# Optimization experiments

Hardware: AMD Instinct MI355X
Metric: run time of the kernel (lower is better)

The kernel has to match this reference:

```python
import jax, jax.numpy as jnp
import numpy as np

N_NODES = 50000
N_EDGES = 600000
HIDDEN = 128


def _sage_conv(x, src, dst, W_l, W_r, b):
    """PyG SAGEConv with mean aggregation:
    out_i = W_l @ mean_{j in N(i)} x_j + W_r @ x_i + b
    src/dst: [E] edge endpoints (message flows src -> dst).
    """
    msg = x[src]  # [E, d] gather
    agg = jax.ops.segment_sum(msg, dst, num_segments=N_NODES)  # [N, d]
    cnt = jax.ops.segment_sum(jnp.ones((src.shape[0],), x.dtype), dst,
                              num_segments=N_NODES)  # [N]
    mean = agg / jnp.maximum(cnt, 1.0)[:, None]
    return mean @ W_l.T + x @ W_r.T + b


def setup_inputs() -> dict:
    key = jax.random.key(0)
    ks = jax.random.split(key, 12)
    x = jax.random.normal(ks[0], (N_NODES, HIDDEN), dtype=jnp.float32)
    edge_index = jax.random.randint(ks[1], (2, N_EDGES), 0, N_NODES, dtype=jnp.int64)
    scale = 1.0 / np.sqrt(HIDDEN)
    inp = {"x": x, "edge_index": edge_index}
    for i, layer in enumerate(["1", "2", "3"]):
        inp["Wl" + layer] = jax.random.uniform(ks[2 + 3 * i], (HIDDEN, HIDDEN),
                                               minval=-scale, maxval=scale, dtype=jnp.float32)
        inp["Wr" + layer] = jax.random.uniform(ks[3 + 3 * i], (HIDDEN, HIDDEN),
                                               minval=-scale, maxval=scale, dtype=jnp.float32)
        inp["b" + layer] = jax.random.uniform(ks[4 + 3 * i], (HIDDEN,),
                                              minval=-scale, maxval=scale, dtype=jnp.float32)
    return inp


def reference(x, edge_index, Wl1, Wr1, b1, Wl2, Wr2, b2, Wl3, Wr3, b3):
    src, dst = edge_index[0], edge_index[1]
    h = jax.nn.relu(_sage_conv(x, src, dst, Wl1, Wr1, b1))
    h = _sage_conv(h, src, dst, Wl2, Wr2, b2)
    h = _sage_conv(h, src, dst, Wl3, Wr3, b3)
    return h
```

## Files before the change

### kernel.cpp

```cpp
#include <hip/hip_runtime.h>
#include <hip/hip_bf16.h>

#define N_NODES 50000
#define N_EDGES 600000
#define HID 128

typedef __attribute__((ext_vector_type(8))) short s8v;
typedef __attribute__((ext_vector_type(8))) unsigned short u8v;
typedef __attribute__((ext_vector_type(4))) float f4v;

__device__ __forceinline__ unsigned short f2bf(float x) {
    unsigned u = __float_as_uint(x);
    unsigned r = u + 0x7FFFu + ((u >> 16) & 1u);
    return (unsigned short)(r >> 16);
}
__device__ __forceinline__ float bf2f(unsigned short u) {
    return __uint_as_float((unsigned)u << 16);
}
__device__ __forceinline__ void split_bf(float x, unsigned short& hi, unsigned short& lo) {
    hi = f2bf(x);
    lo = f2bf(x - bf2f(hi));
}

__device__ __forceinline__ int detect_m64(const void* edges) {
    const int* p = (const int*)edges;
    int lane = threadIdx.x & 63;
    unsigned long long nz = __ballot(p[2 * lane + 1] != 0);
    return (nz == 0ULL) ? 1 : 0;
}

__device__ __forceinline__ int edge_at(const void* edges, int mode64, long long idx) {
    return mode64 ? (int)((const long long*)edges)[idx] : ((const int*)edges)[idx];
}

__global__ __launch_bounds__(256) void prep(
    const void* __restrict__ edges, const float* __restrict__ x,
    const float* __restrict__ m0, const float* __restrict__ m1,
    const float* __restrict__ m2, const float* __restrict__ m3,
    const float* __restrict__ m4, const float* __restrict__ m5,
    int* __restrict__ deg,
    unsigned short* __restrict__ whi, unsigned short* __restrict__ wlo,
    unsigned short* __restrict__ xhi, unsigned short* __restrict__ xlo) {
    const int EB  = (N_EDGES + 255) / 256;
    const int WCV = (6 * HID * HID + 255) / 256;
    const int b = blockIdx.x;
    if (b < EB) {
        int m = detect_m64(edges);
        int e = b * 256 + threadIdx.x;
        if (e >= N_EDGES) return;
        int d = edge_at(edges, m, (long long)N_EDGES + e);
        if ((unsigned)d < (unsigned)N_NODES) atomicAdd(&deg[d], 1);
    } else if (b < EB + WCV) {
        int idx = (b - EB) * 256 + threadIdx.x;
        if (idx >= 6 * HID * HID) return;
        int mat = idx >> 14, off = idx & 16383;
        const float* src = mat == 0 ? m0 : mat == 1 ? m1 : mat == 2 ? m2
                         : mat == 3 ? m3 : mat == 4 ? m4 : m5;
        unsigned short h, l;
        split_bf(src[off], h, l);
        whi[idx] = h; wlo[idx] = l;
    } else {
        const int n4 = (N_NODES * HID) / 4;
        int i = (b - EB - WCV) * 256 + threadIdx.x;
        if (i >= n4) return;
        float4 v = ((const float4*)x)[i];
        ushort4 h, l;
        split_bf(v.x, h.x, l.x);
        split_bf(v.y, h.y, l.y);
        split_bf(v.z, h.z, l.z);
        split_bf(v.w, h.w, l.w);
        ((ushort4*)xhi)[i] = h;
        ((ushort4*)xlo)[i] = l;
    }
}

__global__ void scan_block(const int* __restrict__ deg, int* __restrict__ offs,
                           int* __restrict__ blocksum) {
    __shared__ int sm[256];
    int i = blockIdx.x * 256 + threadIdx.x;
    int v = (i < N_NODES) ? deg[i] : 0;
    sm[threadIdx.x] = v;
    __syncthreads();
    #pragma unroll
    for (int s = 1; s < 256; s <<= 1) {
        int t = (threadIdx.x >= (unsigned)s) ? sm[threadIdx.x - s] : 0;
        __syncthreads();
        sm[threadIdx.x] += t;
        __syncthreads();
    }
    if (i < N_NODES) offs[i] = sm[threadIdx.x] - v;
    if (threadIdx.x == 255) blocksum[blockIdx.x] = sm[255];
}

__global__ void scan_add(int* __restrict__ offs, int* __restrict__ cursor,
                         const int* __restrict__ blocksum, int nblocks) {
    __shared__ int sm[256];
    int t = threadIdx.x;
    int bv = (t < nblocks) ? blocksum[t] : 0;
    sm[t] = (t < (int)blockIdx.x) ? bv : 0;
    __syncthreads();
    #pragma unroll
    for (int s = 128; s > 0; s >>= 1) {
        if (t < s) sm[t] += sm[t + s];
        __syncthreads();
    }
    int prefix = sm[0];
    int i = blockIdx.x * 256 + t;
    if (i < N_NODES) {
        int o = offs[i] + prefix;
        offs[i] = o;
        cursor[i] = o;
    }
    if ((int)blockIdx.x == nblocks - 1 && t == 0)
        offs[N_NODES] = prefix + blocksum[nblocks - 1];
}

__global__ void fill_csr(const void* __restrict__ edges,
                         int* __restrict__ cursor, int* __restrict__ csr) {
    int m = detect_m64(edges);
    int e = blockIdx.x * 256 + threadIdx.x;
    if (e >= N_EDGES) return;
    int d = edge_at(edges, m, (long long)N_EDGES + e);
    int s = edge_at(edges, m, (long long)e);
    if ((unsigned)d >= (unsigned)N_NODES || (unsigned)s >= (unsigned)N_NODES) return;
    int pos = atomicAdd(&cursor[d], 1);
    csr[pos] = s;
}

__global__ __launch_bounds__(256) void aggregate_bf16(const unsigned short* __restrict__ h,
                                                      const int* __restrict__ offs,
                                                      const int* __restrict__ csr,
                                                      unsigned short* __restrict__ mhi,
                                                      unsigned short* __restrict__ mlo) {
    const int sub  = threadIdx.x & 15;
    const int node = blockIdx.x * 16 + (threadIdx.x >> 4);
    if (node >= N_NODES) return;
    const int beg = offs[node], end = offs[node + 1];
    float a[8] = {0.f, 0.f, 0.f, 0.f, 0.f, 0.f, 0.f, 0.f};
    int p = beg;
    for (; p + 8 <= end; p += 8) {
        int s0 = csr[p],     s1 = csr[p + 1], s2 = csr[p + 2], s3 = csr[p + 3];
        int s4 = csr[p + 4], s5 = csr[p + 5], s6 = csr[p + 6], s7 = csr[p + 7];
        u8v v0 = *(const u8v*)(h + (size_t)s0 * HID + sub * 8);
        u8v v1 = *(const u8v*)(h + (size_t)s1 * HID + sub * 8);
        u8v v2 = *(const u8v*)(h + (size_t)s2 * HID + sub * 8);
        u8v v3 = *(const u8v*)(h + (size_t)s3 * HID + sub * 8);
        u8v v4 = *(const u8v*)(h + (size_t)s4 * HID + sub * 8);
        u8v v5 = *(const u8v*)(h + (size_t)s5 * HID + sub * 8);
        u8v v6 = *(const u8v*)(h + (size_t)s6 * HID + sub * 8);
        u8v v7 = *(const u8v*)(h + (size_t)s7 * HID + sub * 8);
        #pragma unroll
        for (int j = 0; j < 8; ++j)
            a[j] += ((bf2f(v0[j]) + bf2f(v1[j])) + (bf2f(v2[j]) + bf2f(v3[j])))
                  + ((bf2f(v4[j]) + bf2f(v5[j])) + (bf2f(v6[j]) + bf2f(v7[j])));
    }
    if (p + 4 <= end) {
        int s0 = csr[p], s1 = csr[p + 1], s2 = csr[p + 2], s3 = csr[p + 3];
        u8v v0 = *(const u8v*)(h + (size_t)s0 * HID + sub * 8);
        u8v v1 = *(const u8v*)(h + (size_t)s1 * HID + sub * 8);
        u8v v2 = *(const u8v*)(h + (size_t)s2 * HID + sub * 8);
        u8v v3 = *(const u8v*)(h + (size_t)s3 * HID + sub * 8);
        #pragma unroll
        for (int j = 0; j < 8; ++j)
            a[j] += (bf2f(v0[j]) + bf2f(v1[j])) + (bf2f(v2[j]) + bf2f(v3[j]));
        p += 4;
    }
    for (; p < end; ++p) {
        int s = csr[p];
        u8v v = *(const u8v*)(h + (size_t)s * HID + sub * 8);
        #pragma unroll
        for (int j = 0; j < 8; ++j) a[j] += bf2f(v[j]);
    }
    const float inv = 1.0f / fmaxf((float)(end - beg), 1.0f);
    u8v hh, ll;
    #pragma unroll
    for (int j = 0; j < 8; ++j) {
        unsigned short hj, lj;
        split_bf(a[j] * inv, hj, lj);
        hh[j] = hj; ll[j] = lj;
    }
    *(u8v*)(mhi + (size_t)node * HID + sub * 8) = hh;
    *(u8v*)(mlo + (size_t)node * HID + sub * 8) = ll;
}

template <int RELU, int FINAL>
__global__ __launch_bounds__(256) void sage_mfma(
    const unsigned short* __restrict__ Mhi, const unsigned short* __restrict__ Mlo,
    const unsigned short* __restrict__ Hhi, const unsigned short* __restrict__ Hlo,
    const unsigned short* __restrict__ Whi, const unsigned short* __restrict__ Wlo,
    const float* __restrict__ bias,
    unsigned short* __restrict__ ohi, unsigned short* __restrict__ olo,
    float* __restrict__ of32) {
    __shared__ short BhS[128 * 72];
    __shared__ short BlS[128 * 72];
    const int tid = threadIdx.x;
    const int wave = tid >> 6, lane = tid & 63;
    const int mIdx = lane & 15, q = lane >> 4;
    const int wrow = (wave & 1) * 64, wcol = (wave >> 1) * 64;
    const int rowBase = blockIdx.x * 128;

    size_t aoff[4];
    #pragma unroll
    for (int t = 0; t < 4; ++t) {
        int node = rowBase + wrow + t * 16 + mIdx;
        if (node > N_NODES - 1) node = N_NODES - 1;
        aoff[t] = (size_t)node * HID + q * 8;
    }

    const int bcol = tid & 127;
    const int bseg = (tid >> 7) * 32;

    f4v acc[4][4];
    #pragma unroll
    for (int a = 0; a < 4; ++a)
        #pragma unroll
        for (int b = 0; b < 4; ++b) acc[a][b] = (f4v){0.f, 0.f, 0.f, 0.f};

    s8v Ah[2][4], Al[2][4];
    auto loadA = [&](int i, int buf) {
        const unsigned short* ah_ = (i < 4) ? Mhi : Hhi;
        const unsigned short* al_ = (i < 4) ? Mlo : Hlo;
        const int kc = (i & 3) * 32;
        #pragma unroll
        for (int t = 0; t < 4; ++t) {
            Ah[buf][t] = *(const s8v*)(ah_ + aoff[t] + kc);
            Al[buf][t] = *(const s8v*)(al_ + aoff[t] + kc);
        }
    };

    loadA(0, 0);
    for (int panel = 0; panel < 4; ++panel) {
        const int ph = panel >> 1;
        const int kb = (panel & 1) * 64;
        const unsigned short* Wh_ = Whi + ph * HID * HID;
        const unsigned short* Wl_ = Wlo + ph * HID * HID;
        __syncthreads();
        {
            const unsigned short* sh = Wh_ + bcol * HID + kb + bseg;
            const unsigned short* sl = Wl_ + bcol * HID + kb + bseg;
            short* dh = BhS + bcol * 72 + bseg;
            short* dl = BlS + bcol * 72 + bseg;
            #pragma unroll
            for (int j = 0; j < 4; ++j) {
                *(s8v*)(dh + j * 8) = *(const s8v*)(sh + j * 8);
                *(s8v*)(dl + j * 8) = *(const s8v*)(sl + j * 8);
            }
        }
        __syncthreads();
        #pragma unroll
        for (int c = 0; c < 2; ++c) {
            const int i = panel * 2 + c;
            if (i < 7) loadA(i + 1, (i + 1) & 1);
            const int kc2 = c * 32;
            s8v Bh_f[4], Bl_f[4];
            #pragma unroll
            for (int nt = 0; nt < 4; ++nt) {
                const int a = (wcol + nt * 16 + mIdx) * 72 + kc2 + q * 8;
                Bh_f[nt] = *(const s8v*)(BhS + a);
                Bl_f[nt] = *(const s8v*)(BlS + a);
            }
            const int buf = i & 1;
            #pragma unroll
            for (int mt = 0; mt < 4; ++mt)
                #pragma unroll
                for (int nt = 0; nt < 4; ++nt) {
                    acc[mt][nt] = __builtin_amdgcn_mfma_f32_16x16x32_bf16(
                        Ah[buf][mt], Bh_f[nt], acc[mt][nt], 0, 0, 0);
                    acc[mt][nt] = __builtin_amdgcn_mfma_f32_16x16x32_bf16(
                        Al[buf][mt], Bh_f[nt], acc[mt][nt], 0, 0, 0);
                    acc[mt][nt] = __builtin_amdgcn_mfma_f32_16x16x32_bf16(
                        Ah[buf][mt], Bl_f[nt], acc[mt][nt], 0, 0, 0);
                }
        }
    }

    float bv[4];
    #pragma unroll
    for (int nt = 0; nt < 4; ++nt) bv[nt] = bias[wcol + nt * 16 + mIdx];

    #pragma unroll
    for (int mt = 0; mt < 4; ++mt)
        #pragma unroll
        for (int r = 0; r < 4; ++r) {
            int node = rowBase + wrow + mt * 16 + q * 4 + r;
            if (node < N_NODES) {
                #pragma unroll
                for (int nt = 0; nt < 4; ++nt) {
                    int feat = wcol + nt * 16 + mIdx;
                    float v = acc[mt][nt][r] + bv[nt];
                    if (RELU) v = fmaxf(v, 0.f);
                    size_t oidx = (size_t)node * HID + feat;
                    if (FINAL) {
                        of32[oidx] = v;
                    } else {
                        unsigned short hh, ll;
                        split_bf(v, hh, ll);
                        ohi[oidx] = hh;
                        olo[oidx] = ll;
                    }
                }
            }
        }
}

extern "C" void kernel_launch(void* const* d_in, const int* in_sizes, int n_in,
                              void* d_out, int out_size, void* d_ws, size_t ws_size,
                              hipStream_t stream) {
    const float* x   = (const float*)d_in[0];
    const void* edges = d_in[1];
    const float* Wl1 = (const float*)d_in[2];
    const float* Wr1 = (const float*)d_in[3];
    const float* b1  = (const float*)d_in[4];
    const float* Wl2 = (const float*)d_in[5];
    const float* Wr2 = (const float*)d_in[6];
    const float* b2  = (const float*)d_in[7];
    const float* Wl3 = (const float*)d_in[8];
    const float* Wr3 = (const float*)d_in[9];
    const float* b3  = (const float*)d_in[10];
    float* out = (float*)d_out;

    char* ws = (char*)d_ws;
    size_t off = 0;
    auto alloc = [&](size_t bytes) -> void* {
        void* p = (void*)(ws + off);
        off += (bytes + 255) & ~(size_t)255;
        return p;
    };
    typedef unsigned short u16;
    const size_t FEAT = (size_t)N_NODES * HID;
    int* deg      = (int*)alloc((size_t)N_NODES * 4);
    int* offs     = (int*)alloc((size_t)(N_NODES + 1) * 4);
    int* cursor   = (int*)alloc((size_t)N_NODES * 4);
    int* blocksum = (int*)alloc(256 * 4);
    int* csr      = (int*)alloc((size_t)N_EDGES * 4);
    u16* whi      = (u16*)alloc((size_t)6 * HID * HID * 2);
    u16* wlo      = (u16*)alloc((size_t)6 * HID * HID * 2);
    u16* xhi      = (u16*)alloc(FEAT * 2);
    u16* xlo      = (u16*)alloc(FEAT * 2);
    u16* h1hi     = (u16*)alloc(FEAT * 2);
    u16* h1lo     = (u16*)alloc(FEAT * 2);
    u16* mhi      = (u16*)alloc(FEAT * 2);
    u16* mlo      = (u16*)alloc(FEAT * 2);
    (void)ws_size; (void)in_sizes; (void)n_in; (void)out_size;

    const int EB    = (N_EDGES + 255) / 256;
    const int NB    = (N_NODES + 255) / 256;
    const int WCV   = (6 * HID * HID + 255) / 256;
    const int XSP   = ((int)(FEAT / 4) + 255) / 256;
    const int PREPB = EB + WCV + XSP;
    const int AGG_B = (N_NODES + 15) / 16;
    const int GEMM_B = (N_NODES + 127) / 128;

    hipMemsetAsync(deg, 0, (size_t)N_NODES * 4, stream);
    prep<<<PREPB, 256, 0, stream>>>(edges, x, Wl1, Wr1, Wl2, Wr2, Wl3, Wr3,
                                    deg, whi, wlo, xhi, xlo);
    scan_block<<<NB, 256, 0, stream>>>(deg, offs, blocksum);
    scan_add<<<NB, 256, 0, stream>>>(offs, cursor, blocksum, NB);
    fill_csr<<<EB, 256, 0, stream>>>(edges, cursor, csr);

    aggregate_bf16<<<AGG_B, 256, 0, stream>>>(xhi, offs, csr, mhi, mlo);
    sage_mfma<1, 0><<<GEMM_B, 256, 0, stream>>>(mhi, mlo, xhi, xlo,
        whi, wlo, b1, h1hi, h1lo, (float*)nullptr);
    aggregate_bf16<<<AGG_B, 256, 0, stream>>>(h1hi, offs, csr, mhi, mlo);
    sage_mfma<0, 0><<<GEMM_B, 256, 0, stream>>>(mhi, mlo, h1hi, h1lo,
        whi + 2 * HID * HID, wlo + 2 * HID * HID, b2, xhi, xlo, (float*)nullptr);
    aggregate_bf16<<<AGG_B, 256, 0, stream>>>(xhi, offs, csr, mhi, mlo);
    sage_mfma<0, 1><<<GEMM_B, 256, 0, stream>>>(mhi, mlo, xhi, xlo,
        whi + 4 * HID * HID, wlo + 4 * HID * HID, b3,
        (u16*)nullptr, (u16*)nullptr, out);
}
```

Baseline: 331.7 us.

## Sort nodes by degree for balanced aggregation and predicate edge-loop tails

Adds a degree histogram during the scan and a counting-sort kernel that builds a permutation of nodes grouped by in-degree. The aggregation kernel processes nodes in that order, so each wavefront's 16-lane node groups see similar edge counts and less divergence. The 8/4/1 tail loops are also replaced by one clamped 8-wide loop with 0/1 weights. The cost is an extra kernel launch, and aggregated rows are now written in scattered rather than sequential node order.

```diff
diff --git a/kernel.cpp b/kernel.cpp
--- a/kernel.cpp
+++ b/kernel.cpp
@@ -4,6 +4,7 @@
 #define N_NODES 50000
 #define N_EDGES 600000
 #define HID 128
+#define NBKT 65
 
 typedef __attribute__((ext_vector_type(8))) short s8v;
 typedef __attribute__((ext_vector_type(8))) unsigned short u8v;
@@ -75,12 +76,15 @@
 }
 
 __global__ void scan_block(const int* __restrict__ deg, int* __restrict__ offs,
-                           int* __restrict__ blocksum) {
+                           int* __restrict__ blocksum, int* __restrict__ ghist) {
     __shared__ int sm[256];
+    __shared__ int hist[NBKT];
     int i = blockIdx.x * 256 + threadIdx.x;
     int v = (i < N_NODES) ? deg[i] : 0;
     sm[threadIdx.x] = v;
+    if (threadIdx.x < NBKT) hist[threadIdx.x] = 0;
     __syncthreads();
+    if (i < N_NODES) atomicAdd(&hist[v < NBKT - 1 ? v : NBKT - 1], 1);
     #pragma unroll
     for (int s = 1; s < 256; s <<= 1) {
         int t = (threadIdx.x >= (unsigned)s) ? sm[threadIdx.x - s] : 0;
@@ -90,6 +94,8 @@
     }
     if (i < N_NODES) offs[i] = sm[threadIdx.x] - v;
     if (threadIdx.x == 255) blocksum[blockIdx.x] = sm[255];
+    if (threadIdx.x < NBKT && hist[threadIdx.x])
+        atomicAdd(&ghist[threadIdx.x], hist[threadIdx.x]);
 }
 
 __global__ void scan_add(int* __restrict__ offs, int* __restrict__ cursor,
@@ -113,6 +119,32 @@
     }
     if ((int)blockIdx.x == nblocks - 1 && t == 0)
         offs[N_NODES] = prefix + blocksum[nblocks - 1];
+}
+
+__global__ __launch_bounds__(256) void order_scatter(
+    const int* __restrict__ deg, const int* __restrict__ ghist,
+    int* __restrict__ gcur, int* __restrict__ order) {
+    __shared__ int pre[NBKT];
+    __shared__ int lcnt[NBKT];
+    __shared__ int lbase[NBKT];
+    int t = threadIdx.x;
+    if (t == 0) {
+        int run = 0;
+        for (int b = 0; b < NBKT; ++b) { pre[b] = run; run += ghist[b]; }
+    }
+    if (t < NBKT) lcnt[t] = 0;
+    __syncthreads();
+    int i = blockIdx.x * 256 + t;
+    int bkt = 0, rank = 0;
+    if (i < N_NODES) {
+        int d = deg[i];
+        bkt = d < NBKT - 1 ? d : NBKT - 1;
+        rank = atomicAdd(&lcnt[bkt], 1);
+    }
+    __syncthreads();
+    if (t < NBKT && lcnt[t]) lbase[t] = atomicAdd(&gcur[t], lcnt[t]);
+    __syncthreads();
+    if (i < N_NODES) order[pre[bkt] + lbase[bkt] + rank] = i;
 }
 
 __global__ void fill_csr(const void* __restrict__ edges,
@@ -130,17 +162,23 @@
 __global__ __launch_bounds__(256) void aggregate_bf16(const unsigned short* __restrict__ h,
                                                       const int* __restrict__ offs,
                                                       const int* __restrict__ csr,
+                                                      const int* __restrict__ order,
                                                       unsigned short* __restrict__ mhi,
                                                       unsigned short* __restrict__ mlo) {
-    const int sub  = threadIdx.x & 15;
-    const int node = blockIdx.x * 16 + (threadIdx.x >> 4);
-    if (node >= N_NODES) return;
+    const int sub = threadIdx.x & 15;
+    const int g   = blockIdx.x * 16 + (threadIdx.x >> 4);
+    if (g >= N_NODES) return;
+    const int node = order[g];
     const int beg = offs[node], end = offs[node + 1];
     float a[8] = {0.f, 0.f, 0.f, 0.f, 0.f, 0.f, 0.f, 0.f};
-    int p = beg;
-    for (; p + 8 <= end; p += 8) {
-        int s0 = csr[p],     s1 = csr[p + 1], s2 = csr[p + 2], s3 = csr[p + 3];
-        int s4 = csr[p + 4], s5 = csr[p + 5], s6 = csr[p + 6], s7 = csr[p + 7];
+    const int e1 = end - 1;
+    for (int p = beg; p < end; p += 8) {
+        int i1 = p + 1 < e1 ? p + 1 : e1, i2 = p + 2 < e1 ? p + 2 : e1;
+        int i3 = p + 3 < e1 ? p + 3 : e1, i4 = p + 4 < e1 ? p + 4 : e1;
+        int i5 = p + 5 < e1 ? p + 5 : e1, i6 = p + 6 < e1 ? p + 6 : e1;
+        int i7 = p + 7 < e1 ? p + 7 : e1;
+        int s0 = csr[p],  s1 = csr[i1], s2 = csr[i2], s3 = csr[i3];
+        int s4 = csr[i4], s5 = csr[i5], s6 = csr[i6], s7 = csr[i7];
         u8v v0 = *(const u8v*)(h + (size_t)s0 * HID + sub * 8);
         u8v v1 = *(const u8v*)(h + (size_t)s1 * HID + sub * 8);
         u8v v2 = *(const u8v*)(h + (size_t)s2 * HID + sub * 8);
@@ -149,27 +187,21 @@
         u8v v5 = *(const u8v*)(h + (size_t)s5 * HID + sub * 8);
         u8v v6 = *(const u8v*)(h + (size_t)s6 * HID + sub * 8);
         u8v v7 = *(const u8v*)(h + (size_t)s7 * HID + sub * 8);
+        float w1 = (p + 1 < end) ? 1.f : 0.f, w2 = (p + 2 < end) ? 1.f : 0.f;
+        float w3 = (p + 3 < end) ? 1.f : 0.f, w4 = (p + 4 < end) ? 1.f : 0.f;
+        float w5 = (p + 5 < end) ? 1.f : 0.f, w6 = (p + 6 < end) ? 1.f : 0.f;
+        float w7 = (p + 7 < end) ? 1.f : 0.f;
         #pragma unroll
-        for (int j = 0; j < 8; ++j)
-            a[j] += ((bf2f(v0[j]) + bf2f(v1[j])) + (bf2f(v2[j]) + bf2f(v3[j])))
-                  + ((bf2f(v4[j]) + bf2f(v5[j])) + (bf2f(v6[j]) + bf2f(v7[j])));
-    }
-    if (p + 4 <= end) {
-        int s0 = csr[p], s1 = csr[p + 1], s2 = csr[p + 2], s3 = csr[p + 3];
-        u8v v0 = *(const u8v*)(h + (size_t)s0 * HID + sub * 8);
-        u8v v1 = *(const u8v*)(h + (size_t)s1 * HID + sub * 8);
-        u8v v2 = *(const u8v*)(h + (size_t)s2 * HID + sub * 8);
-        u8v v3 = *(const u8v*)(h + (size_t)s3 * HID + sub * 8);
-        #pragma unroll
-        for (int j = 0; j < 8; ++j)
-            a[j] += (bf2f(v0[j]) + bf2f(v1[j])) + (bf2f(v2[j]) + bf2f(v3[j]));
-        p += 4;
-    }
-    for (; p < end; ++p) {
-        int s = csr[p];
-        u8v v = *(const u8v*)(h + (size_t)s * HID + sub * 8);
-        #pragma unroll
-        for (int j = 0; j < 8; ++j) a[j] += bf2f(v[j]);
+        for (int j = 0; j < 8; ++j) {
+            float t = a[j] + bf2f(v0[j]);
+            t = fmaf(bf2f(v1[j]), w1, t);
+            t = fmaf(bf2f(v2[j]), w2, t);
+            t = fmaf(bf2f(v3[j]), w3, t);
+            t = fmaf(bf2f(v4[j]), w4, t);
+            t = fmaf(bf2f(v5[j]), w5, t);
+            t = fmaf(bf2f(v6[j]), w6, t);
+            a[j] = fmaf(bf2f(v7[j]), w7, t);
+        }
     }
     const float inv = 1.0f / fmaxf((float)(end - beg), 1.0f);
     u8v hh, ll;
@@ -329,9 +361,13 @@
     typedef unsigned short u16;
     const size_t FEAT = (size_t)N_NODES * HID;
     int* deg      = (int*)alloc((size_t)N_NODES * 4);
+    int* ghist    = (int*)alloc(NBKT * 4);
+    int* gcur     = (int*)alloc(NBKT * 4);
+    const size_t ZERO_BYTES = ((size_t)N_NODES * 4 + 255 & ~(size_t)255) + 512 + 512;
     int* offs     = (int*)alloc((size_t)(N_NODES + 1) * 4);
     int* cursor   = (int*)alloc((size_t)N_NODES * 4);
     int* blocksum = (int*)alloc(256 * 4);
+    int* order    = (int*)alloc((size_t)N_NODES * 4);
     int* csr      = (int*)alloc((size_t)N_EDGES * 4);
     u16* whi      = (u16*)alloc((size_t)6 * HID * HID * 2);
     u16* wlo      = (u16*)alloc((size_t)6 * HID * HID * 2);
@@ -351,20 +387,21 @@
     const int AGG_B = (N_NODES + 15) / 16;
     const int GEMM_B = (N_NODES + 127) / 128;
 
-    hipMemsetAsync(deg, 0, (size_t)N_NODES * 4, stream);
+    hipMemsetAsync(deg, 0, ZERO_BYTES, stream);
     prep<<<PREPB, 256, 0, stream>>>(edges, x, Wl1, Wr1, Wl2, Wr2, Wl3, Wr3,
                                     deg, whi, wlo, xhi, xlo);
-    scan_block<<<NB, 256, 0, stream>>>(deg, offs, blocksum);
+    scan_block<<<NB, 256, 0, stream>>>(deg, offs, blocksum, ghist);
     scan_add<<<NB, 256, 0, stream>>>(offs, cursor, blocksum, NB);
+    order_scatter<<<NB, 256, 0, stream>>>(deg, ghist, gcur, order);
     fill_csr<<<EB, 256, 0, stream>>>(edges, cursor, csr);
 
-    aggregate_bf16<<<AGG_B, 256, 0, stream>>>(xhi, offs, csr, mhi, mlo);
+    aggregate_bf16<<<AGG_B, 256, 0, stream>>>(xhi, offs, csr, order, mhi, mlo);
     sage_mfma<1, 0><<<GEMM_B, 256, 0, stream>>>(mhi, mlo, xhi, xlo,
         whi, wlo, b1, h1hi, h1lo, (float*)nullptr);
-    aggregate_bf16<<<AGG_B, 256, 0, stream>>>(h1hi, offs, csr, mhi, mlo);
+    aggregate_bf16<<<AGG_B, 256, 0, stream>>>(h1hi, offs, csr, order, mhi, mlo);
     sage_mfma<0, 0><<<GEMM_B, 256, 0, stream>>>(mhi, mlo, h1hi, h1lo,
         whi + 2 * HID * HID, wlo + 2 * HID * HID, b2, xhi, xlo, (float*)nullptr);
-    aggregate_bf16<<<AGG_B, 256, 0, stream>>>(xhi, offs, csr, mhi, mlo);
+    aggregate_bf16<<<AGG_B, 256, 0, stream>>>(xhi, offs, csr, order, mhi, mlo);
     sage_mfma<0, 1><<<GEMM_B, 256, 0, stream>>>(mhi, mlo, xhi, xlo,
         whi + 4 * HID * HID, wlo + 4 * HID * HID, b3,
         (u16*)nullptr, (u16*)nullptr, out);
```

Measured after the change: 333.7 us. About the same (+0.6%).
